# Kernel optimization log

Measured on AMD Instinct MI355X. Metric: run time of the kernel, lower is better.

## Reference

```python
import jax, jax.numpy as jnp
import numpy as np
from jax import lax

B, T, D = 256, 2048, 128


def setup_inputs() -> dict:
    key = jax.random.key(0)
    ks = jax.random.split(key, 9)
    s = 1.0 / np.sqrt(D)  # roughly Linear default init scale
    return {
        "evidence_seq": jax.random.normal(ks[0], (B, T, D), dtype=jnp.float32),
        "We": jax.random.normal(ks[1], (D, D), dtype=jnp.float32) * s,
        "be": jax.random.normal(ks[2], (D,), dtype=jnp.float32) * s,
        "Wp": jax.random.normal(ks[3], (D, D), dtype=jnp.float32) * s,
        "bp": jax.random.normal(ks[4], (D,), dtype=jnp.float32) * s,
        "Wl": jax.random.normal(ks[5], (D, D), dtype=jnp.float32) * s,
        "bl": jax.random.normal(ks[6], (D,), dtype=jnp.float32) * s,
        "Ww": jax.random.normal(ks[7], (D, D), dtype=jnp.float32) * s,
        "bw": jax.random.normal(ks[8], (D,), dtype=jnp.float32) * s,
    }


def reference(evidence_seq, We, be, Wp, bp, Wl, bl, Ww, bw):
    # Evidence-only projections are independent of the recurrence:
    # compute them as large batched GEMMs (same math as per-step Linear).
    ev_proj = jnp.einsum("btd,ed->bte", evidence_seq, We) + be  # B,T,D
    leak = jax.nn.sigmoid(jnp.einsum("btd,ed->bte", evidence_seq, Wl) + bl)
    write = jax.nn.sigmoid(jnp.einsum("btd,ed->bte", evidence_seq, Ww) + bw)

    def step(belief_prev, inputs):
        e_t, l_t, w_t = inputs  # each B,D
        cand = jnp.tanh(belief_prev @ Wp.T + bp + e_t)
        belief = l_t * belief_prev + w_t * cand
        return belief, belief

    xs = (
        ev_proj.transpose(1, 0, 2),
        leak.transpose(1, 0, 2),
        write.transpose(1, 0, 2),
    )  # T,B,D each
    belief0 = jnp.zeros((evidence_seq.shape[0], Wp.shape[0]), dtype=evidence_seq.dtype)
    _, beliefs = lax.scan(step, belief0, xs)  # T,B,D
    return beliefs.transpose(1, 0, 2)  # B,T,D
```

## Files before the change

### kernel.cpp

```cpp
#include <hip/hip_runtime.h>
#include <hip/hip_bf16.h>
#include <hip/hip_fp16.h>

#define B_ 256
#define T_ 2048
#define D_ 128

typedef __attribute__((ext_vector_type(8))) short bf16x8;
typedef __attribute__((ext_vector_type(4))) float f32x4;
typedef __attribute__((ext_vector_type(4))) unsigned int u32x4;

__device__ __forceinline__ unsigned int bf_rne(float f) {
    unsigned int u = __builtin_bit_cast(unsigned int, f);
    return (u + 0x7FFFu + ((u >> 16) & 1u)) >> 16;
}
__device__ __forceinline__ unsigned int pack_bf2(float lo, float hi) {
    return bf_rne(lo) | (bf_rne(hi) << 16);
}
__device__ __forceinline__ float bf_to_f(unsigned int h) {
    return __builtin_bit_cast(float, h << 16);
}
__device__ __forceinline__ unsigned int pack_h2(float lo, float hi) {
    unsigned int a = (unsigned int)__half_as_ushort(__float2half_rn(lo));
    unsigned int b = (unsigned int)__half_as_ushort(__float2half_rn(hi));
    return a | (b << 16);
}
__device__ __forceinline__ float h_lo(unsigned int g) {
    return __half2float(__ushort_as_half((unsigned short)(g & 0xFFFFu)));
}
__device__ __forceinline__ float h_hi(unsigned int g) {
    return __half2float(__ushort_as_half((unsigned short)(g >> 16)));
}
__device__ __forceinline__ float sigmoid_f(float x) {
    return __builtin_amdgcn_rcpf(1.0f + __expf(-x));
}
__device__ __forceinline__ float tanh_f(float x) {
    return 1.0f - 2.0f * __builtin_amdgcn_rcpf(__expf(2.0f * x) + 1.0f);
}

__device__ __forceinline__ bf16x8 load_w_frag(const float* __restrict__ W, int row, int dbase) {
    const float4 a = *(const float4*)(W + row * D_ + dbase);
    const float4 b = *(const float4*)(W + row * D_ + dbase + 4);
    union { bf16x8 v; unsigned int u[4]; } r;
    r.u[0] = pack_bf2(a.x, a.y);
    r.u[1] = pack_bf2(a.z, a.w);
    r.u[2] = pack_bf2(b.x, b.y);
    r.u[3] = pack_bf2(b.z, b.w);
    return r.v;
}

__global__ __launch_bounds__(512, 4) void proj_kernel(
    const float* __restrict__ ev,
    const float* __restrict__ We, const float* __restrict__ be,
    const float* __restrict__ Wl, const float* __restrict__ bl,
    const float* __restrict__ Ww, const float* __restrict__ bw,
    const float* __restrict__ bp,
    float* __restrict__ P, unsigned int* __restrict__ G)
{
    __shared__ __align__(16) unsigned short evs[16 * 136];

    const int tid  = threadIdx.x;
    const int wave = tid >> 6, lane = tid & 63;
    const int l15  = lane & 15, quad = lane >> 4;
    const int ebase = wave << 4;
    const int ecol  = ebase + (quad << 2);

    bf16x8 aWe[4], aWl[4], aWw[4];
#pragma unroll
    for (int k = 0; k < 4; ++k) {
        const int dbase = k * 32 + quad * 8;
        aWe[k] = load_w_frag(We, ebase + l15, dbase);
        aWl[k] = load_w_frag(Wl, ebase + l15, dbase);
        aWw[k] = load_w_frag(Ww, ebase + l15, dbase);
    }
    float biasP[4], biasL[4], biasW[4];
#pragma unroll
    for (int r = 0; r < 4; ++r) {
        const int e = ecol + r;
        biasP[r] = be[e] + bp[e];
        biasL[r] = bl[e];
        biasW[r] = bw[e];
    }

    const int srow = tid >> 5;
    const int sd   = (tid & 31) << 2;
    const int NT   = (B_ * T_) / 16;

    int tile = blockIdx.x;
    float4 stg = {0.f, 0.f, 0.f, 0.f};
    if (tile < NT)
        stg = *(const float4*)(ev + (size_t)(tile * 16 + srow) * D_ + sd);

    for (; tile < NT; tile += gridDim.x) {
        *(uint2*)&evs[srow * 136 + sd] =
            make_uint2(pack_bf2(stg.x, stg.y), pack_bf2(stg.z, stg.w));
        __syncthreads();
        const int nt = tile + gridDim.x;
        if (nt < NT)
            stg = *(const float4*)(ev + (size_t)(nt * 16 + srow) * D_ + sd);

        f32x4 accP = {biasP[0], biasP[1], biasP[2], biasP[3]};
        f32x4 accL = {biasL[0], biasL[1], biasL[2], biasL[3]};
        f32x4 accW = {biasW[0], biasW[1], biasW[2], biasW[3]};
#pragma unroll
        for (int k = 0; k < 4; ++k) {
            const bf16x8 bfrag = *(const bf16x8*)&evs[l15 * 136 + k * 32 + quad * 8];
            accP = __builtin_amdgcn_mfma_f32_16x16x32_bf16(aWe[k], bfrag, accP, 0, 0, 0);
            accL = __builtin_amdgcn_mfma_f32_16x16x32_bf16(aWl[k], bfrag, accL, 0, 0, 0);
            accW = __builtin_amdgcn_mfma_f32_16x16x32_bf16(aWw[k], bfrag, accW, 0, 0, 0);
        }
        __syncthreads();

        const size_t row_g = (size_t)tile * 16 + l15;
        *(f32x4*)(P + row_g * D_ + ecol) = accP;
        u32x4 gv;
#pragma unroll
        for (int r = 0; r < 4; ++r)
            gv[r] = pack_h2(sigmoid_f(accL[r]), sigmoid_f(accW[r]));
        *(u32x4*)(G + row_g * D_ + ecol) = gv;
    }
}

__device__ __forceinline__ void chain_step(
    const bf16x8 (&aW0)[4], const bf16x8 (&aW1)[4],
    bf16x8 (&fhi)[4], bf16x8 (&flo)[4],
    f32x4& P0r, f32x4& P1r, u32x4& G0r, u32x4& G1r,
    f32x4& bold0, f32x4& bold1,
    const float* __restrict__ p0, const float* __restrict__ p1,
    const unsigned int* __restrict__ g0, const unsigned int* __restrict__ g1,
    float* __restrict__ o0, float* __restrict__ o1,
    unsigned short* bhi, unsigned short* blo,
    int t, int lw0, int lr, int quad)
{
    f32x4 acc0 = P0r, acc1 = P1r;
    const u32x4 ga = G0r, gb = G1r;
    if (t + 2 < T_) {
        P0r = *(const f32x4*)(p0 + (size_t)(t + 2) * D_);
        P1r = *(const f32x4*)(p1 + (size_t)(t + 2) * D_);
        G0r = *(const u32x4*)(g0 + (size_t)(t + 2) * D_);
        G1r = *(const u32x4*)(g1 + (size_t)(t + 2) * D_);
    }
#pragma unroll
    for (int k = 0; k < 4; ++k) {
        acc0 = __builtin_amdgcn_mfma_f32_16x16x32_bf16(aW0[k], fhi[k], acc0, 0, 0, 0);
        acc1 = __builtin_amdgcn_mfma_f32_16x16x32_bf16(aW1[k], fhi[k], acc1, 0, 0, 0);
    }
#pragma unroll
    for (int k = 0; k < 4; ++k) {
        acc0 = __builtin_amdgcn_mfma_f32_16x16x32_bf16(aW0[k], flo[k], acc0, 0, 0, 0);
        acc1 = __builtin_amdgcn_mfma_f32_16x16x32_bf16(aW1[k], flo[k], acc1, 0, 0, 0);
    }

    f32x4 bn0, bn1;
    unsigned int hh0[4], ll0[4], hh1[4], ll1[4];
#pragma unroll
    for (int r = 0; r < 4; ++r) {
        const float th0 = tanh_f(acc0[r]);
        const float v0  = h_lo(ga[r]) * bold0[r] + h_hi(ga[r]) * th0;
        bn0[r] = v0;
        const unsigned int h0 = bf_rne(v0);
        hh0[r] = h0;
        ll0[r] = bf_rne(v0 - bf_to_f(h0));

        const float th1 = tanh_f(acc1[r]);
        const float v1  = h_lo(gb[r]) * bold1[r] + h_hi(gb[r]) * th1;
        bn1[r] = v1;
        const unsigned int h1 = bf_rne(v1);
        hh1[r] = h1;
        ll1[r] = bf_rne(v1 - bf_to_f(h1));
    }
    bold0 = bn0;
    bold1 = bn1;
    *(f32x4*)(o0 + (size_t)t * D_) = bn0;
    *(f32x4*)(o1 + (size_t)t * D_) = bn1;

    *(uint2*)&bhi[lw0]      = make_uint2(hh0[0] | (hh0[1] << 16), hh0[2] | (hh0[3] << 16));
    *(uint2*)&bhi[lw0 + 16] = make_uint2(hh1[0] | (hh1[1] << 16), hh1[2] | (hh1[3] << 16));
    *(uint2*)&blo[lw0]      = make_uint2(ll0[0] | (ll0[1] << 16), ll0[2] | (ll0[3] << 16));
    *(uint2*)&blo[lw0 + 16] = make_uint2(ll1[0] | (ll1[1] << 16), ll1[2] | (ll1[3] << 16));

    asm volatile("s_waitcnt lgkmcnt(0)\n\ts_barrier" ::: "memory");

#pragma unroll
    for (int k = 0; k < 4; ++k) {
        fhi[k] = *(const bf16x8*)&bhi[lr + k * 32 + quad * 8];
        flo[k] = *(const bf16x8*)&blo[lr + k * 32 + quad * 8];
    }
}

__global__ __launch_bounds__(256) void chain_kernel(
    const float* __restrict__ Wp,
    const unsigned int* __restrict__ G,
    float* __restrict__ Out)
{
    __shared__ __align__(16) unsigned short bl_hi[2][16 * 136];
    __shared__ __align__(16) unsigned short bl_lo[2][16 * 136];

    const int tid  = threadIdx.x;
    const int wave = tid >> 6, lane = tid & 63;
    const int l15  = lane & 15, quad = lane >> 4;
    const int e0   = (wave << 5) + (quad << 2);
    const int b    = (blockIdx.x << 4) + l15;

    bf16x8 aW0[4], aW1[4];
#pragma unroll
    for (int k = 0; k < 4; ++k) {
        const int dbase = k * 32 + quad * 8;
        aW0[k] = load_w_frag(Wp, (wave << 5) + l15, dbase);
        aW1[k] = load_w_frag(Wp, (wave << 5) + 16 + l15, dbase);
    }

    const size_t srow = (size_t)b * T_ * D_;
    const float*        __restrict__ p0 = Out + srow + e0;
    const float*        __restrict__ p1 = Out + srow + e0 + 16;
    const unsigned int* __restrict__ g0 = G   + srow + e0;
    const unsigned int* __restrict__ g1 = G   + srow + e0 + 16;
    float*              __restrict__ o0 = Out + srow + e0;
    float*              __restrict__ o1 = Out + srow + e0 + 16;

    f32x4 Pa0 = *(const f32x4*)(p0);
    f32x4 Pa1 = *(const f32x4*)(p1);
    u32x4 Ga0 = *(const u32x4*)(g0);
    u32x4 Ga1 = *(const u32x4*)(g1);
    f32x4 Pb0 = *(const f32x4*)(p0 + D_);
    f32x4 Pb1 = *(const f32x4*)(p1 + D_);
    u32x4 Gb0 = *(const u32x4*)(g0 + D_);
    u32x4 Gb1 = *(const u32x4*)(g1 + D_);

    bf16x8 fhi[4], flo[4];
#pragma unroll
    for (int k = 0; k < 4; ++k) { fhi[k] = (bf16x8)0; flo[k] = (bf16x8)0; }
    f32x4 bold0 = {0.f, 0.f, 0.f, 0.f};
    f32x4 bold1 = {0.f, 0.f, 0.f, 0.f};

    const int lw0 = l15 * 136 + e0;
    const int lr  = l15 * 136;

    for (int t = 0; t < T_; t += 2) {
        chain_step(aW0, aW1, fhi, flo, Pa0, Pa1, Ga0, Ga1, bold0, bold1,
                   p0, p1, g0, g1, o0, o1,
                   &bl_hi[1][0], &bl_lo[1][0], t, lw0, lr, quad);
        chain_step(aW0, aW1, fhi, flo, Pb0, Pb1, Gb0, Gb1, bold0, bold1,
                   p0, p1, g0, g1, o0, o1,
                   &bl_hi[0][0], &bl_lo[0][0], t + 1, lw0, lr, quad);
    }
}

extern "C" void kernel_launch(void* const* d_in, const int* in_sizes, int n_in,
                              void* d_out, int out_size, void* d_ws, size_t ws_size,
                              hipStream_t stream)
{
    const float* ev = (const float*)d_in[0];
    const float* We = (const float*)d_in[1];
    const float* be = (const float*)d_in[2];
    const float* Wp = (const float*)d_in[3];
    const float* bp = (const float*)d_in[4];
    const float* Wl = (const float*)d_in[5];
    const float* bl = (const float*)d_in[6];
    const float* Ww = (const float*)d_in[7];
    const float* bw = (const float*)d_in[8];
    float* out = (float*)d_out;
    unsigned int* G = (unsigned int*)d_ws;
    (void)in_sizes; (void)n_in; (void)out_size; (void)ws_size;

    proj_kernel<<<1024, 512, 0, stream>>>(ev, We, be, Wl, bl, Ww, bw, bp, out, G);
    chain_kernel<<<16, 256, 0, stream>>>(Wp, G, out);
}
```

Before: 3.109 ms.

## Split recurrence across 8 waves with independent MFMA accumulators

The recurrent chain kernel now uses 512 threads per block, so each wave owns 16 output features instead of 32. This halves the per-wave MFMA chain and the elementwise work per step. The MFMA chain is also split into four independent accumulators summed at the end, which shortens the dependent latency on the critical path. bf16 hi/lo splitting now uses packed hardware conversion. The projection kernel grid is doubled as well, which risks being inconsistent with its tiling loop. More waves per barrier also raise the synchronisation cost on each timestep.

New measurement: 2.957 ms. 1.05x faster.

```diff
diff --git a/kernel.cpp b/kernel.cpp
--- a/kernel.cpp
+++ b/kernel.cpp
@@ -17,8 +17,8 @@
 __device__ __forceinline__ unsigned int pack_bf2(float lo, float hi) {
     return bf_rne(lo) | (bf_rne(hi) << 16);
 }
-__device__ __forceinline__ float bf_to_f(unsigned int h) {
-    return __builtin_bit_cast(float, h << 16);
+__device__ __forceinline__ float bits_as_f(unsigned int u) {
+    return __builtin_bit_cast(float, u);
 }
 __device__ __forceinline__ unsigned int pack_h2(float lo, float hi) {
     unsigned int a = (unsigned int)__half_as_ushort(__float2half_rn(lo));
@@ -36,6 +36,11 @@
 }
 __device__ __forceinline__ float tanh_f(float x) {
     return 1.0f - 2.0f * __builtin_amdgcn_rcpf(__expf(2.0f * x) + 1.0f);
+}
+__device__ __forceinline__ unsigned int cvt_pk_bf16(float a, float b) {
+    union { __hip_bfloat162 h; unsigned int u; } r;
+    r.h = __float22bfloat162_rn(make_float2(a, b));
+    return r.u;
 }
 
 __device__ __forceinline__ bf16x8 load_w_frag(const float* __restrict__ W, int row, int dbase) {
@@ -122,62 +127,54 @@
 }
 
 __device__ __forceinline__ void chain_step(
-    const bf16x8 (&aW0)[4], const bf16x8 (&aW1)[4],
+    const bf16x8 (&aW)[4],
     bf16x8 (&fhi)[4], bf16x8 (&flo)[4],
-    f32x4& P0r, f32x4& P1r, u32x4& G0r, u32x4& G1r,
-    f32x4& bold0, f32x4& bold1,
-    const float* __restrict__ p0, const float* __restrict__ p1,
-    const unsigned int* __restrict__ g0, const unsigned int* __restrict__ g1,
-    float* __restrict__ o0, float* __restrict__ o1,
+    f32x4& Pr, u32x4& Gr,
+    f32x4& bold,
+    const float* __restrict__ p0,
+    const unsigned int* __restrict__ g0,
+    float* __restrict__ o0,
     unsigned short* bhi, unsigned short* blo,
     int t, int lw0, int lr, int quad)
 {
-    f32x4 acc0 = P0r, acc1 = P1r;
-    const u32x4 ga = G0r, gb = G1r;
+    f32x4 a0 = Pr;
+    f32x4 a1 = {0.f, 0.f, 0.f, 0.f};
+    f32x4 a2 = {0.f, 0.f, 0.f, 0.f};
+    f32x4 a3 = {0.f, 0.f, 0.f, 0.f};
+    const u32x4 g = Gr;
     if (t + 2 < T_) {
-        P0r = *(const f32x4*)(p0 + (size_t)(t + 2) * D_);
-        P1r = *(const f32x4*)(p1 + (size_t)(t + 2) * D_);
-        G0r = *(const u32x4*)(g0 + (size_t)(t + 2) * D_);
-        G1r = *(const u32x4*)(g1 + (size_t)(t + 2) * D_);
-    }
-#pragma unroll
-    for (int k = 0; k < 4; ++k) {
-        acc0 = __builtin_amdgcn_mfma_f32_16x16x32_bf16(aW0[k], fhi[k], acc0, 0, 0, 0);
-        acc1 = __builtin_amdgcn_mfma_f32_16x16x32_bf16(aW1[k], fhi[k], acc1, 0, 0, 0);
-    }
-#pragma unroll
-    for (int k = 0; k < 4; ++k) {
-        acc0 = __builtin_amdgcn_mfma_f32_16x16x32_bf16(aW0[k], flo[k], acc0, 0, 0, 0);
-        acc1 = __builtin_amdgcn_mfma_f32_16x16x32_bf16(aW1[k], flo[k], acc1, 0, 0, 0);
-    }
-
-    f32x4 bn0, bn1;
-    unsigned int hh0[4], ll0[4], hh1[4], ll1[4];
+        Pr = *(const f32x4*)(p0 + (size_t)(t + 2) * D_);
+        Gr = *(const u32x4*)(g0 + (size_t)(t + 2) * D_);
+    }
+    a0 = __builtin_amdgcn_mfma_f32_16x16x32_bf16(aW[0], fhi[0], a0, 0, 0, 0);
+    a1 = __builtin_amdgcn_mfma_f32_16x16x32_bf16(aW[1], fhi[1], a1, 0, 0, 0);
+    a2 = __builtin_amdgcn_mfma_f32_16x16x32_bf16(aW[2], fhi[2], a2, 0, 0, 0);
+    a3 = __builtin_amdgcn_mfma_f32_16x16x32_bf16(aW[3], fhi[3], a3, 0, 0, 0);
+    a0 = __builtin_amdgcn_mfma_f32_16x16x32_bf16(aW[0], flo[0], a0, 0, 0, 0);
+    a1 = __builtin_amdgcn_mfma_f32_16x16x32_bf16(aW[1], flo[1], a1, 0, 0, 0);
+    a2 = __builtin_amdgcn_mfma_f32_16x16x32_bf16(aW[2], flo[2], a2, 0, 0, 0);
+    a3 = __builtin_amdgcn_mfma_f32_16x16x32_bf16(aW[3], flo[3], a3, 0, 0, 0);
+    const f32x4 acc = (a0 + a1) + (a2 + a3);
+
+    f32x4 bn;
 #pragma unroll
     for (int r = 0; r < 4; ++r) {
-        const float th0 = tanh_f(acc0[r]);
-        const float v0  = h_lo(ga[r]) * bold0[r] + h_hi(ga[r]) * th0;
-        bn0[r] = v0;
-        const unsigned int h0 = bf_rne(v0);
-        hh0[r] = h0;
-        ll0[r] = bf_rne(v0 - bf_to_f(h0));
-
-        const float th1 = tanh_f(acc1[r]);
-        const float v1  = h_lo(gb[r]) * bold1[r] + h_hi(gb[r]) * th1;
-        bn1[r] = v1;
-        const unsigned int h1 = bf_rne(v1);
-        hh1[r] = h1;
-        ll1[r] = bf_rne(v1 - bf_to_f(h1));
-    }
-    bold0 = bn0;
-    bold1 = bn1;
-    *(f32x4*)(o0 + (size_t)t * D_) = bn0;
-    *(f32x4*)(o1 + (size_t)t * D_) = bn1;
-
-    *(uint2*)&bhi[lw0]      = make_uint2(hh0[0] | (hh0[1] << 16), hh0[2] | (hh0[3] << 16));
-    *(uint2*)&bhi[lw0 + 16] = make_uint2(hh1[0] | (hh1[1] << 16), hh1[2] | (hh1[3] << 16));
-    *(uint2*)&blo[lw0]      = make_uint2(ll0[0] | (ll0[1] << 16), ll0[2] | (ll0[3] << 16));
-    *(uint2*)&blo[lw0 + 16] = make_uint2(ll1[0] | (ll1[1] << 16), ll1[2] | (ll1[3] << 16));
+        const float th = tanh_f(acc[r]);
+        bn[r] = h_lo(g[r]) * bold[r] + h_hi(g[r]) * th;
+    }
+    bold = bn;
+    *(f32x4*)(o0 + (size_t)t * D_) = bn;
+
+    const unsigned int h0 = cvt_pk_bf16(bn[0], bn[1]);
+    const unsigned int h1 = cvt_pk_bf16(bn[2], bn[3]);
+    const float f0 = bits_as_f(h0 << 16);
+    const float f1 = bits_as_f(h0 & 0xFFFF0000u);
+    const float f2 = bits_as_f(h1 << 16);
+    const float f3 = bits_as_f(h1 & 0xFFFF0000u);
+    const unsigned int l0 = cvt_pk_bf16(bn[0] - f0, bn[1] - f1);
+    const unsigned int l1 = cvt_pk_bf16(bn[2] - f2, bn[3] - f3);
+    *(uint2*)&bhi[lw0] = make_uint2(h0, h1);
+    *(uint2*)&blo[lw0] = make_uint2(l0, l1);
 
     asm volatile("s_waitcnt lgkmcnt(0)\n\ts_barrier" ::: "memory");
 
@@ -188,7 +185,7 @@
     }
 }
 
-__global__ __launch_bounds__(256) void chain_kernel(
+__global__ __launch_bounds__(512) void chain_kernel(
     const float* __restrict__ Wp,
     const unsigned int* __restrict__ G,
     float* __restrict__ Out)
@@ -199,49 +196,36 @@
     const int tid  = threadIdx.x;
     const int wave = tid >> 6, lane = tid & 63;
     const int l15  = lane & 15, quad = lane >> 4;
-    const int e0   = (wave << 5) + (quad << 2);
+    const int e0   = (wave << 4) + (quad << 2);
     const int b    = (blockIdx.x << 4) + l15;
 
-    bf16x8 aW0[4], aW1[4];
-#pragma unroll
-    for (int k = 0; k < 4; ++k) {
-        const int dbase = k * 32 + quad * 8;
-        aW0[k] = load_w_frag(Wp, (wave << 5) + l15, dbase);
-        aW1[k] = load_w_frag(Wp, (wave << 5) + 16 + l15, dbase);
-    }
+    bf16x8 aW[4];
+#pragma unroll
+    for (int k = 0; k < 4; ++k)
+        aW[k] = load_w_frag(Wp, (wave << 4) + l15, k * 32 + quad * 8);
 
     const size_t srow = (size_t)b * T_ * D_;
     const float*        __restrict__ p0 = Out + srow + e0;
-    const float*        __restrict__ p1 = Out + srow + e0 + 16;
     const unsigned int* __restrict__ g0 = G   + srow + e0;
-    const unsigned int* __restrict__ g1 = G   + srow + e0 + 16;
     float*              __restrict__ o0 = Out + srow + e0;
-    float*              __restrict__ o1 = Out + srow + e0 + 16;
-
-    f32x4 Pa0 = *(const f32x4*)(p0);
-    f32x4 Pa1 = *(const f32x4*)(p1);
-    u32x4 Ga0 = *(const u32x4*)(g0);
-    u32x4 Ga1 = *(const u32x4*)(g1);
-    f32x4 Pb0 = *(const f32x4*)(p0 + D_);
-    f32x4 Pb1 = *(const f32x4*)(p1 + D_);
-    u32x4 Gb0 = *(const u32x4*)(g0 + D_);
-    u32x4 Gb1 = *(const u32x4*)(g1 + D_);
+
+    f32x4 Pa = *(const f32x4*)(p0);
+    u32x4 Ga = *(const u32x4*)(g0);
+    f32x4 Pb = *(const f32x4*)(p0 + D_);
+    u32x4 Gb = *(const u32x4*)(g0 + D_);
 
     bf16x8 fhi[4], flo[4];
 #pragma unroll
     for (int k = 0; k < 4; ++k) { fhi[k] = (bf16x8)0; flo[k] = (bf16x8)0; }
-    f32x4 bold0 = {0.f, 0.f, 0.f, 0.f};
-    f32x4 bold1 = {0.f, 0.f, 0.f, 0.f};
+    f32x4 bold = {0.f, 0.f, 0.f, 0.f};
 
     const int lw0 = l15 * 136 + e0;
     const int lr  = l15 * 136;
 
     for (int t = 0; t < T_; t += 2) {
-        chain_step(aW0, aW1, fhi, flo, Pa0, Pa1, Ga0, Ga1, bold0, bold1,
-                   p0, p1, g0, g1, o0, o1,
+        chain_step(aW, fhi, flo, Pa, Ga, bold, p0, g0, o0,
                    &bl_hi[1][0], &bl_lo[1][0], t, lw0, lr, quad);
-        chain_step(aW0, aW1, fhi, flo, Pb0, Pb1, Gb0, Gb1, bold0, bold1,
-                   p0, p1, g0, g1, o0, o1,
+        chain_step(aW, fhi, flo, Pb, Gb, bold, p0, g0, o0,
                    &bl_hi[0][0], &bl_lo[0][0], t + 1, lw0, lr, quad);
     }
 }
@@ -263,6 +247,6 @@
     unsigned int* G = (unsigned int*)d_ws;
     (void)in_sizes; (void)n_in; (void)out_size; (void)ws_size;
 
-    proj_kernel<<<1024, 512, 0, stream>>>(ev, We, be, Wl, bl, Ww, bw, bp, out, G);
-    chain_kernel<<<16, 256, 0, stream>>>(Wp, G, out);
-}
+    proj_kernel<<<2048, 512, 0, stream>>>(ev, We, be, Wl, bl, Ww, bw, bp, out, G);
+    chain_kernel<<<16, 512, 0, stream>>>(Wp, G, out);
+}
```
